# Optimization experiments

Measured on AMD Instinct MI355X. Metric: run time of the kernel, lower is better.

The kernel has to match this reference:

```python
import jax, jax.numpy as jnp
import numpy as np

VOCAB = 30000
EMB = 128
ENC = 128
BS = 256
DEPTH = 10            # perfect binary tree depth
N = 2 ** DEPTH - 1    # 1023 nodes per tree, heap layout: children of i are 2i+1, 2i+2


def setup_inputs() -> dict:
    key = jax.random.key(0)
    k1, k2, k3, k4 = jax.random.split(key, 4)
    tokens = jax.random.randint(k1, (BS, N), 0, VOCAB)                       # node token ids
    emb = jax.random.normal(k2, (VOCAB, EMB), jnp.float32) * 0.02            # embedding table
    W_c = jax.random.normal(k3, (ENC, EMB), jnp.float32) / np.sqrt(EMB)      # Linear weight [out,in]
    b_c = jax.random.normal(k4, (ENC,), jnp.float32) * 0.01                  # Linear bias
    return {"tokens": tokens, "emb": emb, "W_c": W_c, "b_c": b_c, "bs": BS}


def reference(tokens, emb, W_c, b_c, bs):
    # Per-node leaf contribution: c = W_c(embedding(token))  -> [bs, N, ENC]
    c = jnp.einsum('bne,oe->bno', emb[tokens], W_c) + b_c
    # Bottom-up tree sum: h[i] = c[i] + h[2i+1] + h[2i+2]
    h = c
    for l in reversed(range(DEPTH - 1)):          # fixed small loop over tree depth
        s = 2 ** l - 1
        e = 2 ** (l + 1) - 1
        left = h[:, 2 * s + 1:2 * e:2]            # children of parents [s, e)
        right = h[:, 2 * s + 2:2 * e + 1:2]
        h = h.at[:, s:e].add(left + right)
    # Max-pool over all nodes of each tree (original: max over stacked node_list)
    return jnp.max(h, axis=1)                     # [bs, ENC]
```

## Files before the change

kernel.cpp:

```cpp
#include <hip/hip_runtime.h>
#include <hip/hip_bf16.h>
#include <stdint.h>

#define VOCAB 30000
#define EMB 128
#define ENC 128
#define BS 256
#define NNODES 1023

#define QSCALE 512.0f
#define QINV   (1.0f / 512.0f)

typedef short short8 __attribute__((ext_vector_type(8)));
typedef float f32x4 __attribute__((ext_vector_type(4)));

__device__ __forceinline__ unsigned short f2bf(float x) {
    uint32_t u = __float_as_uint(x);
    uint32_t r = u + 0x7fffu + ((u >> 16) & 1u);
    return (unsigned short)(r >> 16);
}

__device__ __forceinline__ int4 unpack4(uint32_t p) {
    int4 r;
    r.x = (int)(signed char)(p & 0xffu);
    r.y = (int)(signed char)((p >> 8) & 0xffu);
    r.z = (int)(signed char)((p >> 16) & 0xffu);
    r.w = (int)(signed char)(p >> 24);
    return r;
}

#define WLD 136
__global__ void __launch_bounds__(256) project_k(const float* __restrict__ emb,
                                                 const float* __restrict__ W,
                                                 const float* __restrict__ bias,
                                                 signed char* __restrict__ P) {
    __shared__ unsigned short Wlds[ENC * WLD];

    const int wave = threadIdx.x >> 6;
    const int lane = threadIdx.x & 63;
    const int r = lane & 15;
    const int q = lane >> 4;
    const int v0 = blockIdx.x * 64 + wave * 16;

    int vr = v0 + r;
    if (vr > VOCAB - 1) vr = VOCAB - 1;

    const float* erow = emb + (size_t)vr * EMB + q * 8;
    float4 e0[4], e1[4];
#pragma unroll
    for (int kk = 0; kk < 4; kk++) {
        e0[kk] = *(const float4*)(erow + kk * 32);
        e1[kk] = *(const float4*)(erow + kk * 32 + 4);
    }
    float bb[8];
#pragma unroll
    for (int ot = 0; ot < 8; ot++) bb[ot] = bias[ot * 16 + r];

    for (int i = threadIdx.x; i < (ENC * EMB) / 4; i += 256) {
        const int e = i * 4;
        const int o = e >> 7, k = e & 127;
        const float4 x = *(const float4*)(W + e);
        ushort4 s;
        s.x = f2bf(x.x); s.y = f2bf(x.y); s.z = f2bf(x.z); s.w = f2bf(x.w);
        *(ushort4*)(Wlds + o * WLD + k) = s;
    }
    __syncthreads();

    short8 af[4];
#pragma unroll
    for (int kk = 0; kk < 4; kk++) {
        short8 a;
        a[0] = (short)f2bf(e0[kk].x); a[1] = (short)f2bf(e0[kk].y);
        a[2] = (short)f2bf(e0[kk].z); a[3] = (short)f2bf(e0[kk].w);
        a[4] = (short)f2bf(e1[kk].x); a[5] = (short)f2bf(e1[kk].y);
        a[6] = (short)f2bf(e1[kk].z); a[7] = (short)f2bf(e1[kk].w);
        af[kk] = a;
    }

#pragma unroll
    for (int ot = 0; ot < 8; ot++) {
        const int o0 = ot * 16;
        f32x4 acc = {0.f, 0.f, 0.f, 0.f};
        const unsigned short* wrow = Wlds + (o0 + r) * WLD + q * 8;
#pragma unroll
        for (int kk = 0; kk < 4; kk++) {
            short8 bf = *(const short8*)(wrow + kk * 32);
            acc = __builtin_amdgcn_mfma_f32_16x16x32_bf16(af[kk], bf, acc, 0, 0, 0);
        }
        const float bbv = bb[ot];
#pragma unroll
        for (int i = 0; i < 4; i++) {
            const int vo = v0 + q * 4 + i;
            if (vo < VOCAB) {
                const float x = fminf(fmaxf((acc[i] + bbv) * QSCALE, -127.0f), 127.0f);
                P[(size_t)vo * ENC + o0 + r] = (signed char)__float2int_rn(x);
            }
        }
    }
}

__global__ void __launch_bounds__(512) tree_k(const int* __restrict__ tokens,
                                              const signed char* __restrict__ P,
                                              float* __restrict__ out) {
    __shared__ int s_tok[NNODES + 1];
    __shared__ int s_sum[32][ENC];
    __shared__ int s_max[32][ENC];

    const int b    = blockIdx.x;
    const int* tb  = tokens + b * NNODES;

    for (int i = threadIdx.x; i < NNODES; i += 512) s_tok[i] = tb[i];
    __syncthreads();

    const int lane = threadIdx.x & 63;
    const int w    = threadIdx.x >> 6;
    const int half = lane >> 5;
    const int c    = lane & 31;
    const uint32_t* Pw = (const uint32_t*)P;

#pragma unroll 1
    for (int pr = 0; pr < 2; pr++) {
        const int st  = w * 4 + pr * 2 + half;
        const int rp1 = 32 + st;

        int4 m4; m4.x = m4.y = m4.z = m4.w = -(1 << 30);

        int4 v[16];
        {
            const int base = (rp1 << 4) - 1;
#pragma unroll
            for (int i = 0; i < 16; i++)
                v[i] = unpack4(Pw[(size_t)s_tok[base + i] * 32 + c]);
#pragma unroll
            for (int i = 0; i < 16; i++) {
                m4.x = max(m4.x, v[i].x); m4.y = max(m4.y, v[i].y);
                m4.z = max(m4.z, v[i].z); m4.w = max(m4.w, v[i].w);
            }
        }
        int4 u[8];
        {
            const int base = (rp1 << 3) - 1;
#pragma unroll
            for (int i = 0; i < 8; i++) {
                const int4 p = unpack4(Pw[(size_t)s_tok[base + i] * 32 + c]);
                u[i].x = p.x + v[2*i].x + v[2*i+1].x;
                u[i].y = p.y + v[2*i].y + v[2*i+1].y;
                u[i].z = p.z + v[2*i].z + v[2*i+1].z;
                u[i].w = p.w + v[2*i].w + v[2*i+1].w;
                m4.x = max(m4.x, u[i].x); m4.y = max(m4.y, u[i].y);
                m4.z = max(m4.z, u[i].z); m4.w = max(m4.w, u[i].w);
            }
        }
        int4 w4[4];
        {
            const int base = (rp1 << 2) - 1;
#pragma unroll
            for (int i = 0; i < 4; i++) {
                const int4 p = unpack4(Pw[(size_t)s_tok[base + i] * 32 + c]);
                w4[i].x = p.x + u[2*i].x + u[2*i+1].x;
                w4[i].y = p.y + u[2*i].y + u[2*i+1].y;
                w4[i].z = p.z + u[2*i].z + u[2*i+1].z;
                w4[i].w = p.w + u[2*i].w + u[2*i+1].w;
                m4.x = max(m4.x, w4[i].x); m4.y = max(m4.y, w4[i].y);
                m4.z = max(m4.z, w4[i].z); m4.w = max(m4.w, w4[i].w);
            }
        }
        int4 z[2];
        {
            const int base = (rp1 << 1) - 1;
#pragma unroll
            for (int i = 0; i < 2; i++) {
                const int4 p = unpack4(Pw[(size_t)s_tok[base + i] * 32 + c]);
                z[i].x = p.x + w4[2*i].x + w4[2*i+1].x;
                z[i].y = p.y + w4[2*i].y + w4[2*i+1].y;
                z[i].z = p.z + w4[2*i].z + w4[2*i+1].z;
                z[i].w = p.w + w4[2*i].w + w4[2*i+1].w;
                m4.x = max(m4.x, z[i].x); m4.y = max(m4.y, z[i].y);
                m4.z = max(m4.z, z[i].z); m4.w = max(m4.w, z[i].w);
            }
        }
        {
            const int4 p = unpack4(Pw[(size_t)s_tok[rp1 - 1] * 32 + c]);
            int4 s;
            s.x = p.x + z[0].x + z[1].x;
            s.y = p.y + z[0].y + z[1].y;
            s.z = p.z + z[0].z + z[1].z;
            s.w = p.w + z[0].w + z[1].w;
            m4.x = max(m4.x, s.x); m4.y = max(m4.y, s.y);
            m4.z = max(m4.z, s.z); m4.w = max(m4.w, s.w);
            ((int4*)s_sum[st])[c] = s;
            ((int4*)s_max[st])[c] = m4;
        }
    }

    __syncthreads();
    if (threadIdx.x >= ENC) return;
    const int ch = threadIdx.x;

    int m = -(1 << 30);
    int vv[32];
#pragma unroll
    for (int i = 0; i < 32; i++) vv[i] = s_sum[i][ch];
#pragma unroll
    for (int i = 0; i < 32; i++) m = max(m, s_max[i][ch]);

    int uu[16];
#pragma unroll
    for (int i = 0; i < 16; i++) {
        uu[i] = (int)P[(size_t)s_tok[15 + i] * ENC + ch] + vv[2 * i] + vv[2 * i + 1];
        m = max(m, uu[i]);
    }
    int w8[8];
#pragma unroll
    for (int i = 0; i < 8; i++) {
        w8[i] = (int)P[(size_t)s_tok[7 + i] * ENC + ch] + uu[2 * i] + uu[2 * i + 1];
        m = max(m, w8[i]);
    }
    int w4[4];
#pragma unroll
    for (int i = 0; i < 4; i++) {
        w4[i] = (int)P[(size_t)s_tok[3 + i] * ENC + ch] + w8[2 * i] + w8[2 * i + 1];
        m = max(m, w4[i]);
    }
    int w2[2];
#pragma unroll
    for (int i = 0; i < 2; i++) {
        w2[i] = (int)P[(size_t)s_tok[1 + i] * ENC + ch] + w4[2 * i] + w4[2 * i + 1];
        m = max(m, w2[i]);
    }
    const int s0 = (int)P[(size_t)s_tok[0] * ENC + ch] + w2[0] + w2[1];
    m = max(m, s0);

    out[b * ENC + ch] = (float)m * QINV;
}

extern "C" void kernel_launch(void* const* d_in, const int* in_sizes, int n_in,
                              void* d_out, int out_size, void* d_ws, size_t ws_size,
                              hipStream_t stream) {
    const int*   tokens = (const int*)d_in[0];
    const float* emb    = (const float*)d_in[1];
    const float* W_c    = (const float*)d_in[2];
    const float* b_c    = (const float*)d_in[3];
    float* out = (float*)d_out;

    signed char* P = (signed char*)d_ws;

    project_k<<<(VOCAB + 63) / 64, 256, 0, stream>>>(emb, W_c, b_c, P);
    tree_k<<<BS, 512, 0, stream>>>(tokens, P, out);
}
```

Measured before the change: 83.78 us.

## Pack int8 projection stores and issue all subtree gathers up front with 1024 threads

The projection kernel swaps the MFMA operand order so each lane holds four consecutive output channels. It then packs them into one 32-bit store instead of four scattered byte stores. The tree kernel uses 1024 threads so each half-wave handles a single subtree, with no serial two-pass loop. It also issues all 31 gathers before any arithmetic and precomputes row offsets in shared memory, which exposes more memory-level parallelism at the cost of more registers per thread.

```diff
diff --git a/kernel.cpp b/kernel.cpp
--- a/kernel.cpp
+++ b/kernel.cpp
@@ -29,6 +29,16 @@
     return r;
 }
 
+__device__ __forceinline__ int4 add4(int4 a, int4 b) {
+    int4 r; r.x = a.x + b.x; r.y = a.y + b.y; r.z = a.z + b.z; r.w = a.w + b.w;
+    return r;
+}
+
+__device__ __forceinline__ void max4(int4& m, int4 a) {
+    m.x = max(m.x, a.x); m.y = max(m.y, a.y);
+    m.z = max(m.z, a.z); m.w = max(m.w, a.w);
+}
+
 #define WLD 136
 __global__ void __launch_bounds__(256) project_k(const float* __restrict__ emb,
                                                  const float* __restrict__ W,
@@ -42,6 +52,7 @@
     const int q = lane >> 4;
     const int v0 = blockIdx.x * 64 + wave * 16;
 
+    const bool vr_ok = (v0 + r) < VOCAB;
     int vr = v0 + r;
     if (vr > VOCAB - 1) vr = VOCAB - 1;
 
@@ -52,9 +63,9 @@
         e0[kk] = *(const float4*)(erow + kk * 32);
         e1[kk] = *(const float4*)(erow + kk * 32 + 4);
     }
-    float bb[8];
-#pragma unroll
-    for (int ot = 0; ot < 8; ot++) bb[ot] = bias[ot * 16 + r];
+    float4 bv[8];
+#pragma unroll
+    for (int ot = 0; ot < 8; ot++) bv[ot] = *(const float4*)(bias + ot * 16 + q * 4);
 
     for (int i = threadIdx.x; i < (ENC * EMB) / 4; i += 256) {
         const int e = i * 4;
@@ -77,6 +88,8 @@
         af[kk] = a;
     }
 
+    uint32_t* Prow = (uint32_t*)(P + (size_t)vr * ENC);
+
 #pragma unroll
     for (int ot = 0; ot < 8; ot++) {
         const int o0 = ot * 16;
@@ -85,31 +98,35 @@
 #pragma unroll
         for (int kk = 0; kk < 4; kk++) {
             short8 bf = *(const short8*)(wrow + kk * 32);
-            acc = __builtin_amdgcn_mfma_f32_16x16x32_bf16(af[kk], bf, acc, 0, 0, 0);
+            acc = __builtin_amdgcn_mfma_f32_16x16x32_bf16(bf, af[kk], acc, 0, 0, 0);
         }
-        const float bbv = bb[ot];
-#pragma unroll
-        for (int i = 0; i < 4; i++) {
-            const int vo = v0 + q * 4 + i;
-            if (vo < VOCAB) {
-                const float x = fminf(fmaxf((acc[i] + bbv) * QSCALE, -127.0f), 127.0f);
-                P[(size_t)vo * ENC + o0 + r] = (signed char)__float2int_rn(x);
-            }
+        const float4 bb = bv[ot];
+        uint32_t pack = 0;
+        {
+            float x0 = fminf(fmaxf((acc[0] + bb.x) * QSCALE, -127.0f), 127.0f);
+            float x1 = fminf(fmaxf((acc[1] + bb.y) * QSCALE, -127.0f), 127.0f);
+            float x2 = fminf(fmaxf((acc[2] + bb.z) * QSCALE, -127.0f), 127.0f);
+            float x3 = fminf(fmaxf((acc[3] + bb.w) * QSCALE, -127.0f), 127.0f);
+            pack  = ((uint32_t)(__float2int_rn(x0) & 0xff));
+            pack |= ((uint32_t)(__float2int_rn(x1) & 0xff)) << 8;
+            pack |= ((uint32_t)(__float2int_rn(x2) & 0xff)) << 16;
+            pack |= ((uint32_t)(__float2int_rn(x3) & 0xff)) << 24;
         }
-    }
-}
-
-__global__ void __launch_bounds__(512) tree_k(const int* __restrict__ tokens,
-                                              const signed char* __restrict__ P,
-                                              float* __restrict__ out) {
-    __shared__ int s_tok[NNODES + 1];
+        if (vr_ok) Prow[ot * 4 + q] = pack;
+    }
+}
+
+__global__ void __launch_bounds__(1024) tree_k(const int* __restrict__ tokens,
+                                               const signed char* __restrict__ P,
+                                               float* __restrict__ out) {
+    __shared__ int s_off[NNODES + 1];
     __shared__ int s_sum[32][ENC];
     __shared__ int s_max[32][ENC];
 
     const int b    = blockIdx.x;
     const int* tb  = tokens + b * NNODES;
 
-    for (int i = threadIdx.x; i < NNODES; i += 512) s_tok[i] = tb[i];
+    if (threadIdx.x < NNODES) s_off[threadIdx.x] = tb[threadIdx.x] << 5;
     __syncthreads();
 
     const int lane = threadIdx.x & 63;
@@ -118,79 +135,58 @@
     const int c    = lane & 31;
     const uint32_t* Pw = (const uint32_t*)P;
 
-#pragma unroll 1
-    for (int pr = 0; pr < 2; pr++) {
-        const int st  = w * 4 + pr * 2 + half;
-        const int rp1 = 32 + st;
-
-        int4 m4; m4.x = m4.y = m4.z = m4.w = -(1 << 30);
-
-        int4 v[16];
-        {
-            const int base = (rp1 << 4) - 1;
-#pragma unroll
-            for (int i = 0; i < 16; i++)
-                v[i] = unpack4(Pw[(size_t)s_tok[base + i] * 32 + c]);
-#pragma unroll
-            for (int i = 0; i < 16; i++) {
-                m4.x = max(m4.x, v[i].x); m4.y = max(m4.y, v[i].y);
-                m4.z = max(m4.z, v[i].z); m4.w = max(m4.w, v[i].w);
-            }
-        }
-        int4 u[8];
-        {
-            const int base = (rp1 << 3) - 1;
-#pragma unroll
-            for (int i = 0; i < 8; i++) {
-                const int4 p = unpack4(Pw[(size_t)s_tok[base + i] * 32 + c]);
-                u[i].x = p.x + v[2*i].x + v[2*i+1].x;
-                u[i].y = p.y + v[2*i].y + v[2*i+1].y;
-                u[i].z = p.z + v[2*i].z + v[2*i+1].z;
-                u[i].w = p.w + v[2*i].w + v[2*i+1].w;
-                m4.x = max(m4.x, u[i].x); m4.y = max(m4.y, u[i].y);
-                m4.z = max(m4.z, u[i].z); m4.w = max(m4.w, u[i].w);
-            }
-        }
-        int4 w4[4];
-        {
-            const int base = (rp1 << 2) - 1;
-#pragma unroll
-            for (int i = 0; i < 4; i++) {
-                const int4 p = unpack4(Pw[(size_t)s_tok[base + i] * 32 + c]);
-                w4[i].x = p.x + u[2*i].x + u[2*i+1].x;
-                w4[i].y = p.y + u[2*i].y + u[2*i+1].y;
-                w4[i].z = p.z + u[2*i].z + u[2*i+1].z;
-                w4[i].w = p.w + u[2*i].w + u[2*i+1].w;
-                m4.x = max(m4.x, w4[i].x); m4.y = max(m4.y, w4[i].y);
-                m4.z = max(m4.z, w4[i].z); m4.w = max(m4.w, w4[i].w);
-            }
-        }
-        int4 z[2];
-        {
-            const int base = (rp1 << 1) - 1;
-#pragma unroll
-            for (int i = 0; i < 2; i++) {
-                const int4 p = unpack4(Pw[(size_t)s_tok[base + i] * 32 + c]);
-                z[i].x = p.x + w4[2*i].x + w4[2*i+1].x;
-                z[i].y = p.y + w4[2*i].y + w4[2*i+1].y;
-                z[i].z = p.z + w4[2*i].z + w4[2*i+1].z;
-                z[i].w = p.w + w4[2*i].w + w4[2*i+1].w;
-                m4.x = max(m4.x, z[i].x); m4.y = max(m4.y, z[i].y);
-                m4.z = max(m4.z, z[i].z); m4.w = max(m4.w, z[i].w);
-            }
-        }
-        {
-            const int4 p = unpack4(Pw[(size_t)s_tok[rp1 - 1] * 32 + c]);
-            int4 s;
-            s.x = p.x + z[0].x + z[1].x;
-            s.y = p.y + z[0].y + z[1].y;
-            s.z = p.z + z[0].z + z[1].z;
-            s.w = p.w + z[0].w + z[1].w;
-            m4.x = max(m4.x, s.x); m4.y = max(m4.y, s.y);
-            m4.z = max(m4.z, s.z); m4.w = max(m4.w, s.w);
-            ((int4*)s_sum[st])[c] = s;
-            ((int4*)s_max[st])[c] = m4;
-        }
+    const int st  = w * 2 + half;
+    const int rp1 = 32 + st;
+
+    const int base16 = (rp1 << 4) - 1;
+    const int base8  = (rp1 << 3) - 1;
+    const int base4  = (rp1 << 2) - 1;
+    const int base2  = (rp1 << 1) - 1;
+    uint32_t raw[31];
+#pragma unroll
+    for (int i = 0; i < 16; i++) raw[i]      = Pw[(uint32_t)s_off[base16 + i] + c];
+#pragma unroll
+    for (int i = 0; i < 8; i++)  raw[16 + i] = Pw[(uint32_t)s_off[base8 + i] + c];
+#pragma unroll
+    for (int i = 0; i < 4; i++)  raw[24 + i] = Pw[(uint32_t)s_off[base4 + i] + c];
+#pragma unroll
+    for (int i = 0; i < 2; i++)  raw[28 + i] = Pw[(uint32_t)s_off[base2 + i] + c];
+    raw[30] = Pw[(uint32_t)s_off[rp1 - 1] + c];
+
+    int4 m4; m4.x = m4.y = m4.z = m4.w = -(1 << 30);
+
+    int4 vp[8];
+#pragma unroll
+    for (int i = 0; i < 8; i++) {
+        const int4 a = unpack4(raw[2 * i]);
+        const int4 d = unpack4(raw[2 * i + 1]);
+        max4(m4, a); max4(m4, d);
+        vp[i] = add4(a, d);
+    }
+    int4 up[4];
+#pragma unroll
+    for (int i = 0; i < 4; i++) {
+        const int4 ua = add4(unpack4(raw[16 + 2 * i]), vp[2 * i]);
+        const int4 ub = add4(unpack4(raw[16 + 2 * i + 1]), vp[2 * i + 1]);
+        max4(m4, ua); max4(m4, ub);
+        up[i] = add4(ua, ub);
+    }
+    int4 wp[2];
+#pragma unroll
+    for (int i = 0; i < 2; i++) {
+        const int4 wa = add4(unpack4(raw[24 + 2 * i]), up[2 * i]);
+        const int4 wb = add4(unpack4(raw[24 + 2 * i + 1]), up[2 * i + 1]);
+        max4(m4, wa); max4(m4, wb);
+        wp[i] = add4(wa, wb);
+    }
+    {
+        const int4 za = add4(unpack4(raw[28]), wp[0]);
+        const int4 zb = add4(unpack4(raw[29]), wp[1]);
+        max4(m4, za); max4(m4, zb);
+        const int4 s = add4(unpack4(raw[30]), add4(za, zb));
+        max4(m4, s);
+        ((int4*)s_sum[st])[c] = s;
+        ((int4*)s_max[st])[c] = m4;
     }
 
     __syncthreads();
@@ -207,28 +203,28 @@
     int uu[16];
 #pragma unroll
     for (int i = 0; i < 16; i++) {
-        uu[i] = (int)P[(size_t)s_tok[15 + i] * ENC + ch] + vv[2 * i] + vv[2 * i + 1];
+        uu[i] = (int)P[(size_t)((uint32_t)s_off[15 + i]) * 4 + ch] + vv[2 * i] + vv[2 * i + 1];
         m = max(m, uu[i]);
     }
     int w8[8];
 #pragma unroll
     for (int i = 0; i < 8; i++) {
-        w8[i] = (int)P[(size_t)s_tok[7 + i] * ENC + ch] + uu[2 * i] + uu[2 * i + 1];
+        w8[i] = (int)P[(size_t)((uint32_t)s_off[7 + i]) * 4 + ch] + uu[2 * i] + uu[2 * i + 1];
         m = max(m, w8[i]);
     }
     int w4[4];
 #pragma unroll
     for (int i = 0; i < 4; i++) {
-        w4[i] = (int)P[(size_t)s_tok[3 + i] * ENC + ch] + w8[2 * i] + w8[2 * i + 1];
+        w4[i] = (int)P[(size_t)((uint32_t)s_off[3 + i]) * 4 + ch] + w8[2 * i] + w8[2 * i + 1];
         m = max(m, w4[i]);
     }
     int w2[2];
 #pragma unroll
     for (int i = 0; i < 2; i++) {
-        w2[i] = (int)P[(size_t)s_tok[1 + i] * ENC + ch] + w4[2 * i] + w4[2 * i + 1];
+        w2[i] = (int)P[(size_t)((uint32_t)s_off[1 + i]) * 4 + ch] + w4[2 * i] + w4[2 * i + 1];
         m = max(m, w2[i]);
     }
-    const int s0 = (int)P[(size_t)s_tok[0] * ENC + ch] + w2[0] + w2[1];
+    const int s0 = (int)P[(size_t)((uint32_t)s_off[0]) * 4 + ch] + w2[0] + w2[1];
     m = max(m, s0);
 
     out[b * ENC + ch] = (float)m * QINV;
@@ -246,5 +242,5 @@
     signed char* P = (signed char*)d_ws;
 
     project_k<<<(VOCAB + 63) / 64, 256, 0, stream>>>(emb, W_c, b_c, P);
-    tree_k<<<BS, 512, 0, stream>>>(tokens, P, out);
-}
+    tree_k<<<BS, 1024, 0, stream>>>(tokens, P, out);
+}
```

Result: no change. 83.39 us (-0.5%).
